# Kernel optimization log

Measured on AMD Instinct MI355X. Metric: run time of the kernel, lower is better.

## Reference

```python
import jax, jax.numpy as jnp
import numpy as np

INPUT_SIZE = 256
HIDDEN_SIZE = 512


def setup_inputs() -> dict:
    key = jax.random.key(0)
    ks = jax.random.split(key, 8)
    N, L = 128, 1024
    bound_cell = 1.0 / np.sqrt(HIDDEN_SIZE)
    bound_fc = 1.0 / np.sqrt(HIDDEN_SIZE)
    u = lambda k, shape, b: jax.random.uniform(k, shape, jnp.float32, -b, b)
    return {
        "x": jax.random.normal(ks[0], (N, L, INPUT_SIZE), jnp.float32),
        "h": jnp.zeros((N, HIDDEN_SIZE), jnp.float32),
        "W_ih": u(ks[1], (HIDDEN_SIZE, INPUT_SIZE), bound_cell),
        "W_hh": u(ks[2], (HIDDEN_SIZE, HIDDEN_SIZE), bound_cell),
        "b_ih": u(ks[3], (HIDDEN_SIZE,), bound_cell),
        "b_hh": u(ks[4], (HIDDEN_SIZE,), bound_cell),
        "W_out": u(ks[5], (HIDDEN_SIZE, HIDDEN_SIZE), bound_fc),
        "b_out": u(ks[6], (HIDDEN_SIZE,), bound_fc),
    }


def reference(x, h, W_ih, W_hh, b_ih, b_hh, W_out, b_out):
    # Precompute input projections for all timesteps in one big GEMM: [N,L,H]
    xp = jnp.einsum("nli,hi->nlh", x, W_ih) + b_ih + b_hh

    def step(h, xp_t):
        h = jnp.tanh(xp_t + h @ W_hh.T)
        return h, None

    # scan over time: xp transposed to [L,N,H]
    h, _ = jax.lax.scan(step, h, jnp.swapaxes(xp, 0, 1))
    y = h @ W_out.T + b_out
    return (y, h)
```

## Files before the change

### kernel.cpp

```cpp
#include <hip/hip_runtime.h>

typedef _Float16 f16;
typedef _Float16 f16x2 __attribute__((ext_vector_type(2)));
typedef _Float16 f16x4 __attribute__((ext_vector_type(4)));
typedef _Float16 f16x8 __attribute__((ext_vector_type(8)));
typedef float    f32x4 __attribute__((ext_vector_type(4)));

static __device__ __forceinline__ float dot4(uint4 w, uint4 h, float acc) {
    acc = __builtin_amdgcn_fdot2(__builtin_bit_cast(f16x2, w.x), __builtin_bit_cast(f16x2, h.x), acc, false);
    acc = __builtin_amdgcn_fdot2(__builtin_bit_cast(f16x2, w.y), __builtin_bit_cast(f16x2, h.y), acc, false);
    acc = __builtin_amdgcn_fdot2(__builtin_bit_cast(f16x2, w.z), __builtin_bit_cast(f16x2, h.z), acc, false);
    acc = __builtin_amdgcn_fdot2(__builtin_bit_cast(f16x2, w.w), __builtin_bit_cast(f16x2, h.w), acc, false);
    return acc;
}

static __device__ __forceinline__ float dppx1(float v) {
    int r = __builtin_amdgcn_mov_dpp(__builtin_bit_cast(int, v), 0xB1, 0xF, 0xF, true);
    return __builtin_bit_cast(float, r);
}
static __device__ __forceinline__ float dppx2(float v) {
    int r = __builtin_amdgcn_mov_dpp(__builtin_bit_cast(int, v), 0x4E, 0xF, 0xF, true);
    return __builtin_bit_cast(float, r);
}

__global__ __launch_bounds__(256) void cvt_w(const float4* __restrict__ wih4,
                                             const float4* __restrict__ whh4,
                                             f16x4* __restrict__ wih16,
                                             f16x4* __restrict__ whh16) {
    int idx = blockIdx.x * 256 + threadIdx.x;
    if (idx < 32768) {
        float4 v = wih4[idx];
        wih16[idx] = (f16x4){(f16)v.x, (f16)v.y, (f16)v.z, (f16)v.w};
    } else if (idx < 98304) {
        int k = idx - 32768;
        float4 v = whh4[k];
        whh16[k] = (f16x4){(f16)v.x, (f16)v.y, (f16)v.z, (f16)v.w};
    }
}

__global__ __launch_bounds__(256) void gemm_xp(const float* __restrict__ x,
                                               const f16* __restrict__ wih,
                                               const float* __restrict__ bih,
                                               const float* __restrict__ bhh,
                                               f16* __restrict__ xp,
                                               int tc, int t0, int L) {
    __shared__ f16 As[128][48];
    __shared__ f16 Bs[128][48];
    int tid = threadIdx.x;
    int r = tid >> 1, kh = (tid & 1) * 16;

    long mbase = (long)blockIdx.x * 128;
    int jb = blockIdx.y * 128;
    long mp = mbase + r;
    int n = (int)(mp / tc);
    int trel = (int)(mp - (long)n * tc);
    const float* xrow = x + ((long)n * L + t0 + trel) * 256 + kh;
    const f16* wrow = wih + (jb + r) * 256 + kh;

    int w = tid >> 6, l = tid & 63, lr = l & 15, lk = l >> 4;
    int wm = w & 1, wn = w >> 1;

    f32x4 acc[4][4] = {};

    for (int kk = 0; kk < 256; kk += 32) {
        float4 a0 = *(const float4*)(xrow + kk);
        float4 a1 = *(const float4*)(xrow + kk + 4);
        float4 a2 = *(const float4*)(xrow + kk + 8);
        float4 a3 = *(const float4*)(xrow + kk + 12);
        uint4  b0 = *(const uint4*)(wrow + kk);
        uint4  b1 = *(const uint4*)(wrow + kk + 8);
        f16x8 ca = {(f16)a0.x,(f16)a0.y,(f16)a0.z,(f16)a0.w,(f16)a1.x,(f16)a1.y,(f16)a1.z,(f16)a1.w};
        f16x8 cb = {(f16)a2.x,(f16)a2.y,(f16)a2.z,(f16)a2.w,(f16)a3.x,(f16)a3.y,(f16)a3.z,(f16)a3.w};
        __syncthreads();
        *(f16x8*)&As[r][kh]     = ca;
        *(f16x8*)&As[r][kh + 8] = cb;
        *(uint4*)&Bs[r][kh]     = b0;
        *(uint4*)&Bs[r][kh + 8] = b1;
        __syncthreads();

        uint4 af[4], bf[4];
#pragma unroll
        for (int mi = 0; mi < 4; ++mi) af[mi] = *(const uint4*)&As[wm * 64 + mi * 16 + lr][lk * 8];
#pragma unroll
        for (int ni = 0; ni < 4; ++ni) bf[ni] = *(const uint4*)&Bs[wn * 64 + ni * 16 + lr][lk * 8];
#pragma unroll
        for (int mi = 0; mi < 4; ++mi)
#pragma unroll
            for (int ni = 0; ni < 4; ++ni)
                acc[mi][ni] = __builtin_amdgcn_mfma_f32_16x16x32_f16(
                    __builtin_bit_cast(f16x8, af[mi]), __builtin_bit_cast(f16x8, bf[ni]),
                    acc[mi][ni], 0, 0, 0);
    }

#pragma unroll
    for (int ni = 0; ni < 4; ++ni) {
        int j = jb + wn * 64 + ni * 16 + lr;
        float bias = bih[j] + bhh[j];
#pragma unroll
        for (int mi = 0; mi < 4; ++mi) {
            long row = mbase + wm * 64 + mi * 16 + lk * 4;
#pragma unroll
            for (int rr = 0; rr < 4; ++rr)
                xp[(row + rr) * 512 + j] = (f16)(acc[mi][ni][rr] + bias);
        }
    }
}

__global__ __launch_bounds__(1024) void rnn_seq(const f16* __restrict__ whh16,
                                                const f16* __restrict__ xp,
                                                const float* __restrict__ hin,
                                                float* __restrict__ out,
                                                const float* __restrict__ wout,
                                                const float* __restrict__ bout,
                                                int tc, int finalflag, int ytotal) {
    __shared__ uint4 WL[8192];
    __shared__ uint4 hbuf[2][80];

    const int tid = threadIdx.x;
    const int n = blockIdx.x;
    const int i  = tid & 15;
    const int jg = tid >> 4;
    const int sw = tid & 7;

    uint4 wr[8][3];
    const f16* wbase = whh16 + (long)(jg * 8) * 512 + i * 32;
#pragma unroll
    for (int r = 0; r < 8; ++r) {
        const uint4* p = (const uint4*)(wbase + (long)r * 512);
        wr[r][0] = p[0]; wr[r][1] = p[1]; wr[r][2] = p[2];
        WL[tid * 8 + (r ^ sw)] = p[3];
    }

    if (tid < 512) {
        int j = tid;
        ((f16*)&hbuf[0][0])[((j >> 5) * 5 + ((j >> 3) & 3)) * 8 + (j & 7)] =
            (f16)hin[n * 512 + j];
    }
    __syncthreads();

    const int jrow = ((i & 1) << 2) | (i & 2) | ((i >> 2) & 1);
    const int jfin = jg * 8 + jrow;
    const int widx = ((jfin >> 5) * 5 + ((jfin >> 3) & 3)) * 8 + (jfin & 7);
    const f16* xpp = xp + ((long)n * tc) * 512 + jfin;
    const int wbyte = tid * 128 + sw * 16;

    float lasth = 0.f;
    int cur = 0;

    for (int t = 0; t < tc; ++t) {
        float xv = (float)xpp[(long)t * 512];

        const uint4* hrow = &hbuf[cur][i * 5];
        uint4 hv0 = hrow[0], hv1 = hrow[1], hv2 = hrow[2], hv3 = hrow[3];

        float a[8];
#pragma unroll
        for (int r = 0; r < 8; ++r)
            a[r] = dot4(wr[r][2], hv2, dot4(wr[r][1], hv1, dot4(wr[r][0], hv0, 0.f)));
#pragma unroll
        for (int r = 0; r < 8; ++r) {
            uint4 wl = *(const uint4*)((const char*)WL + (wbyte ^ (r << 4)));
            a[r] = dot4(wl, hv3, a[r]);
        }

#pragma unroll
        for (int s = 0; s < 4; ++s) {
            float lo = a[s], hi = a[s + 4];
            float keep = (i & 1) ? hi : lo, send = (i & 1) ? lo : hi;
            a[s] = keep + dppx1(send);
        }
#pragma unroll
        for (int s = 0; s < 2; ++s) {
            float lo = a[s], hi = a[s + 2];
            float keep = (i & 2) ? hi : lo, send = (i & 2) ? lo : hi;
            a[s] = keep + dppx2(send);
        }
        {
            float lo = a[0], hi = a[1];
            float keep = (i & 4) ? hi : lo, send = (i & 4) ? lo : hi;
            a[0] = keep + __shfl_xor(send, 4);
        }
        a[0] += __shfl_xor(a[0], 8);

        float pre = a[0] + xv;
        pre = fminf(fmaxf(pre, -20.f), 20.f);
        float e = __expf(2.f * pre);
        float hn = 1.f - 2.f / (e + 1.f);
        lasth = hn;
        ((f16*)&hbuf[cur ^ 1][0])[widx] = (f16)hn;
        __syncthreads();
        cur ^= 1;
    }

    out[ytotal + n * 512 + jfin] = lasth;

    if (finalflag) {
        __syncthreads();
        float* hf = (float*)WL;
        hf[jfin] = lasth;
        __syncthreads();
        if (tid < 512) {
            int jy = tid;
            float acc = bout[jy];
            const float* wrp = wout + (long)jy * 512;
#pragma unroll 4
            for (int k = 0; k < 512; k += 8) {
                float4 w0 = *(const float4*)(wrp + k);
                float4 w1 = *(const float4*)(wrp + k + 4);
                float4 g0 = *(const float4*)(hf + k);
                float4 g1 = *(const float4*)(hf + k + 4);
                acc = fmaf(w0.x, g0.x, acc); acc = fmaf(w0.y, g0.y, acc);
                acc = fmaf(w0.z, g0.z, acc); acc = fmaf(w0.w, g0.w, acc);
                acc = fmaf(w1.x, g1.x, acc); acc = fmaf(w1.y, g1.y, acc);
                acc = fmaf(w1.z, g1.z, acc); acc = fmaf(w1.w, g1.w, acc);
            }
            out[n * 512 + jy] = acc;
        }
    }
}

extern "C" void kernel_launch(void* const* d_in, const int* in_sizes, int n_in,
                              void* d_out, int out_size, void* d_ws, size_t ws_size,
                              hipStream_t stream) {
    const float* x    = (const float*)d_in[0];
    const float* h0   = (const float*)d_in[1];
    const float* wih  = (const float*)d_in[2];
    const float* whh  = (const float*)d_in[3];
    const float* bih  = (const float*)d_in[4];
    const float* bhh  = (const float*)d_in[5];
    const float* wout = (const float*)d_in[6];
    const float* bout = (const float*)d_in[7];
    float* out = (float*)d_out;

    int N = in_sizes[1] / 512;
    int L = (int)((long)in_sizes[0] / ((long)N * 256));
    int ytotal = N * 512;

    char* ws = (char*)d_ws;
    f16* whh16 = (f16*)ws;
    f16* wih16 = (f16*)(ws + 524288);
    f16* xp    = (f16*)(ws + 786432);
    long per_t = (long)N * 512 * 2;
    long cap = (ws_size > 786432) ? (long)(ws_size - 786432) : 0;
    long Tc = cap / per_t;
    if (Tc > L) Tc = L;
    if (Tc < 1) Tc = 1;

    cvt_w<<<384, 256, 0, stream>>>((const float4*)wih, (const float4*)whh,
                                   (f16x4*)wih16, (f16x4*)whh16);

    for (int t0 = 0; t0 < L;) {
        int tc = (int)((L - t0 < Tc) ? (L - t0) : Tc);
        gemm_xp<<<dim3(tc, 4), 256, 0, stream>>>(x, wih16, bih, bhh, xp, tc, t0, L);
        const float* hsrc = (t0 == 0) ? h0 : (const float*)(out + ytotal);
        int fin = (t0 + tc == L) ? 1 : 0;
        rnn_seq<<<N, 1024, 0, stream>>>(whh16, xp, hsrc, out, wout, bout, tc, fin, ytotal);
        t0 += tc;
    }
}
```

Before: 1.997 ms.

## Shrink recurrent block to 256 threads with 16 rows per thread group

Each RNN sequence block now runs with 256 threads instead of 1024. Each 8-lane group covers 16 hidden rows, with more W_hh held in registers (96 uint4 per thread) and the remainder in LDS. The reduction tree grows a level, and each lane finishes two outputs with a packed xp load and a packed h store. The aim is cheaper per-step barriers and fewer waves synchronizing. The cost is much higher register pressure that may spill, and less parallelism per step.

```diff
diff --git a/kernel.cpp b/kernel.cpp
--- a/kernel.cpp
+++ b/kernel.cpp
@@ -106,101 +106,111 @@
     }
 }
 
-__global__ __launch_bounds__(1024) void rnn_seq(const f16* __restrict__ whh16,
-                                                const f16* __restrict__ xp,
-                                                const float* __restrict__ hin,
-                                                float* __restrict__ out,
-                                                const float* __restrict__ wout,
-                                                const float* __restrict__ bout,
-                                                int tc, int finalflag, int ytotal) {
+__global__ __launch_bounds__(256, 1) void rnn_seq(const f16* __restrict__ whh16,
+                                                  const f16* __restrict__ xp,
+                                                  const float* __restrict__ hin,
+                                                  float* __restrict__ out,
+                                                  const float* __restrict__ wout,
+                                                  const float* __restrict__ bout,
+                                                  int tc, int finalflag, int ytotal) {
     __shared__ uint4 WL[8192];
-    __shared__ uint4 hbuf[2][80];
+    __shared__ uint4 hb[2][64];
 
     const int tid = threadIdx.x;
     const int n = blockIdx.x;
-    const int i  = tid & 15;
-    const int jg = tid >> 4;
-    const int sw = tid & 7;
-
-    uint4 wr[8][3];
-    const f16* wbase = whh16 + (long)(jg * 8) * 512 + i * 32;
-#pragma unroll
-    for (int r = 0; r < 8; ++r) {
+    const int i  = tid & 7;
+    const int jg = tid >> 3;
+
+    uint4 wr[16][6];
+    const f16* wbase = whh16 + (long)(jg * 16) * 512 + i * 64;
+#pragma unroll
+    for (int r = 0; r < 16; ++r) {
         const uint4* p = (const uint4*)(wbase + (long)r * 512);
-        wr[r][0] = p[0]; wr[r][1] = p[1]; wr[r][2] = p[2];
-        WL[tid * 8 + (r ^ sw)] = p[3];
-    }
-
-    if (tid < 512) {
-        int j = tid;
-        ((f16*)&hbuf[0][0])[((j >> 5) * 5 + ((j >> 3) & 3)) * 8 + (j & 7)] =
-            (f16)hin[n * 512 + j];
+#pragma unroll
+        for (int c = 0; c < 6; ++c) wr[r][c] = p[c];
+        WL[(r * 2 + 0) * 256 + tid] = p[6];
+        WL[(r * 2 + 1) * 256 + tid] = p[7];
+    }
+
+    f16* hb0 = (f16*)&hb[0][0];
+#pragma unroll
+    for (int e = 0; e < 2; ++e) {
+        int j = tid * 2 + e;
+        int g = j >> 6, c = (j >> 3) & 7, p = j & 7;
+        hb0[(g * 8 + (c ^ g)) * 8 + p] = (f16)hin[n * 512 + j];
     }
     __syncthreads();
 
-    const int jrow = ((i & 1) << 2) | (i & 2) | ((i >> 2) & 1);
-    const int jfin = jg * 8 + jrow;
-    const int widx = ((jfin >> 5) * 5 + ((jfin >> 3) & 3)) * 8 + (jfin & 7);
-    const f16* xpp = xp + ((long)n * tc) * 512 + jfin;
-    const int wbyte = tid * 128 + sw * 16;
-
-    float lasth = 0.f;
+    const int jr0 = 8 * (i & 1) + 4 * ((i >> 1) & 1) + 2 * ((i >> 2) & 1);
+    const int j0 = jg * 16 + jr0;
+    const int wg0 = j0 >> 6, wc0 = (j0 >> 3) & 7, wp0 = j0 & 7;
+    const int hwidx = (wg0 * 8 + (wc0 ^ wg0)) * 8 + wp0;
+    const f16* xpp = xp + ((long)n * tc) * 512 + j0;
+
+    float h0f = 0.f, h1f = 0.f;
     int cur = 0;
 
     for (int t = 0; t < tc; ++t) {
-        float xv = (float)xpp[(long)t * 512];
-
-        const uint4* hrow = &hbuf[cur][i * 5];
-        uint4 hv0 = hrow[0], hv1 = hrow[1], hv2 = hrow[2], hv3 = hrow[3];
-
-        float a[8];
-#pragma unroll
-        for (int r = 0; r < 8; ++r)
-            a[r] = dot4(wr[r][2], hv2, dot4(wr[r][1], hv1, dot4(wr[r][0], hv0, 0.f)));
-#pragma unroll
-        for (int r = 0; r < 8; ++r) {
-            uint4 wl = *(const uint4*)((const char*)WL + (wbyte ^ (r << 4)));
-            a[r] = dot4(wl, hv3, a[r]);
-        }
-
+        unsigned xv2 = *(const unsigned*)(xpp + (long)t * 512);
+
+        const uint4* hc = &hb[cur][i * 8];
+        float a[16];
+
+        uint4 h0 = hc[0 ^ i], h1 = hc[1 ^ i], h2 = hc[2 ^ i], h3 = hc[3 ^ i];
+#pragma unroll
+        for (int r = 0; r < 16; ++r)
+            a[r] = dot4(wr[r][3], h3, dot4(wr[r][2], h2, dot4(wr[r][1], h1, dot4(wr[r][0], h0, 0.f))));
+        h0 = hc[4 ^ i]; h1 = hc[5 ^ i]; h2 = hc[6 ^ i]; h3 = hc[7 ^ i];
+#pragma unroll
+        for (int r = 0; r < 16; ++r) {
+            float v = dot4(wr[r][5], h1, dot4(wr[r][4], h0, a[r]));
+            v = dot4(WL[(r * 2 + 0) * 256 + tid], h2, v);
+            a[r] = dot4(WL[(r * 2 + 1) * 256 + tid], h3, v);
+        }
+
+#pragma unroll
+        for (int s = 0; s < 8; ++s) {
+            float lo = a[s], hi = a[s + 8];
+            float keep = (i & 1) ? hi : lo, send = (i & 1) ? lo : hi;
+            a[s] = keep + dppx1(send);
+        }
 #pragma unroll
         for (int s = 0; s < 4; ++s) {
             float lo = a[s], hi = a[s + 4];
-            float keep = (i & 1) ? hi : lo, send = (i & 1) ? lo : hi;
-            a[s] = keep + dppx1(send);
+            float keep = (i & 2) ? hi : lo, send = (i & 2) ? lo : hi;
+            a[s] = keep + dppx2(send);
         }
 #pragma unroll
         for (int s = 0; s < 2; ++s) {
             float lo = a[s], hi = a[s + 2];
-            float keep = (i & 2) ? hi : lo, send = (i & 2) ? lo : hi;
-            a[s] = keep + dppx2(send);
-        }
-        {
-            float lo = a[0], hi = a[1];
             float keep = (i & 4) ? hi : lo, send = (i & 4) ? lo : hi;
-            a[0] = keep + __shfl_xor(send, 4);
-        }
-        a[0] += __shfl_xor(a[0], 8);
-
-        float pre = a[0] + xv;
-        pre = fminf(fmaxf(pre, -20.f), 20.f);
-        float e = __expf(2.f * pre);
-        float hn = 1.f - 2.f / (e + 1.f);
-        lasth = hn;
-        ((f16*)&hbuf[cur ^ 1][0])[widx] = (f16)hn;
+            a[s] = keep + __shfl_xor(send, 4);
+        }
+
+        f16x2 xv = __builtin_bit_cast(f16x2, xv2);
+        float pre0 = a[0] + (float)xv.x;
+        float pre1 = a[1] + (float)xv.y;
+        pre0 = fminf(fmaxf(pre0, -20.f), 20.f);
+        pre1 = fminf(fmaxf(pre1, -20.f), 20.f);
+        h0f = 1.f - 2.f / (__expf(2.f * pre0) + 1.f);
+        h1f = 1.f - 2.f / (__expf(2.f * pre1) + 1.f);
+        f16x2 hx = {(f16)h0f, (f16)h1f};
+        *(f16x2*)&((f16*)&hb[cur ^ 1][0])[hwidx] = hx;
         __syncthreads();
         cur ^= 1;
     }
 
-    out[ytotal + n * 512 + jfin] = lasth;
+    out[ytotal + n * 512 + j0]     = h0f;
+    out[ytotal + n * 512 + j0 + 1] = h1f;
 
     if (finalflag) {
-        __syncthreads();
         float* hf = (float*)WL;
-        hf[jfin] = lasth;
-        __syncthreads();
-        if (tid < 512) {
-            int jy = tid;
+        hf[j0]     = h0f;
+        hf[j0 + 1] = h1f;
+        __syncthreads();
+#pragma unroll
+        for (int e = 0; e < 2; ++e) {
+            int jy = tid + e * 256;
             float acc = bout[jy];
             const float* wrp = wout + (long)jy * 512;
 #pragma unroll 4
@@ -254,7 +264,7 @@
         gemm_xp<<<dim3(tc, 4), 256, 0, stream>>>(x, wih16, bih, bhh, xp, tc, t0, L);
         const float* hsrc = (t0 == 0) ? h0 : (const float*)(out + ytotal);
         int fin = (t0 + tc == L) ? 1 : 0;
-        rnn_seq<<<N, 1024, 0, stream>>>(whh16, xp, hsrc, out, wout, bout, tc, fin, ytotal);
+        rnn_seq<<<N, 256, 0, stream>>>(whh16, xp, hsrc, out, wout, bout, tc, fin, ytotal);
         t0 += tc;
     }
 }
```

New measurement: 3.046 ms. 52.5% more time.

## Halve RNN recurrence block to 512 threads with 8-lane K split

Applied to the files above, without the earlier changes.

The sequential recurrence kernel now uses 512 threads per sequence instead of 1024. Each thread covers 64 of the K dimension: 48 weights per row sit in registers and 16 in LDS, stored in a new transposed layout. This removes one cross-lane reduction stage and makes the per-step barrier cheaper, at the cost of twice the dot-product work per thread and higher register pressure. The h buffer layout changes to an XOR swizzle to avoid LDS bank conflicts.

```diff
diff --git a/kernel.cpp b/kernel.cpp
--- a/kernel.cpp
+++ b/kernel.cpp
@@ -106,43 +106,43 @@
     }
 }
 
-__global__ __launch_bounds__(1024) void rnn_seq(const f16* __restrict__ whh16,
-                                                const f16* __restrict__ xp,
-                                                const float* __restrict__ hin,
-                                                float* __restrict__ out,
-                                                const float* __restrict__ wout,
-                                                const float* __restrict__ bout,
-                                                int tc, int finalflag, int ytotal) {
-    __shared__ uint4 WL[8192];
-    __shared__ uint4 hbuf[2][80];
+__global__ __launch_bounds__(512, 1) void rnn_seq(const f16* __restrict__ whh16,
+                                                  const f16* __restrict__ xp,
+                                                  const float* __restrict__ hin,
+                                                  float* __restrict__ out,
+                                                  const float* __restrict__ wout,
+                                                  const float* __restrict__ bout,
+                                                  int tc, int finalflag, int ytotal) {
+    __shared__ uint4 WL[16 * 512];
+    __shared__ uint4 hb[2][64];
 
     const int tid = threadIdx.x;
     const int n = blockIdx.x;
-    const int i  = tid & 15;
-    const int jg = tid >> 4;
-    const int sw = tid & 7;
-
-    uint4 wr[8][3];
-    const f16* wbase = whh16 + (long)(jg * 8) * 512 + i * 32;
+    const int i  = tid & 7;
+    const int jg = tid >> 3;
+
+    uint4 wr[8][6];
+    const f16* wbase = whh16 + (long)(jg * 8) * 512 + i * 64;
 #pragma unroll
     for (int r = 0; r < 8; ++r) {
         const uint4* p = (const uint4*)(wbase + (long)r * 512);
-        wr[r][0] = p[0]; wr[r][1] = p[1]; wr[r][2] = p[2];
-        WL[tid * 8 + (r ^ sw)] = p[3];
-    }
-
-    if (tid < 512) {
+#pragma unroll
+        for (int c = 0; c < 6; ++c) wr[r][c] = p[c];
+        WL[(r * 2 + 0) * 512 + tid] = p[6];
+        WL[(r * 2 + 1) * 512 + tid] = p[7];
+    }
+
+    {
         int j = tid;
-        ((f16*)&hbuf[0][0])[((j >> 5) * 5 + ((j >> 3) & 3)) * 8 + (j & 7)] =
-            (f16)hin[n * 512 + j];
+        int g = j >> 6, c = (j >> 3) & 7, p = j & 7;
+        ((f16*)&hb[0][0])[(g * 8 + (c ^ g)) * 8 + p] = (f16)hin[n * 512 + j];
     }
     __syncthreads();
 
-    const int jrow = ((i & 1) << 2) | (i & 2) | ((i >> 2) & 1);
-    const int jfin = jg * 8 + jrow;
-    const int widx = ((jfin >> 5) * 5 + ((jfin >> 3) & 3)) * 8 + (jfin & 7);
+    const int jfin = jg * 8 + (((i & 1) << 2) | (i & 2) | ((i >> 2) & 1));
+    const int wg0 = jfin >> 6, wc0 = (jfin >> 3) & 7, wp0 = jfin & 7;
+    const int hwidx = (wg0 * 8 + (wc0 ^ wg0)) * 8 + wp0;
     const f16* xpp = xp + ((long)n * tc) * 512 + jfin;
-    const int wbyte = tid * 128 + sw * 16;
 
     float lasth = 0.f;
     int cur = 0;
@@ -150,17 +150,19 @@
     for (int t = 0; t < tc; ++t) {
         float xv = (float)xpp[(long)t * 512];
 
-        const uint4* hrow = &hbuf[cur][i * 5];
-        uint4 hv0 = hrow[0], hv1 = hrow[1], hv2 = hrow[2], hv3 = hrow[3];
-
+        const uint4* hc = &hb[cur][i * 8];
         float a[8];
+
+        uint4 h0 = hc[0 ^ i], h1 = hc[1 ^ i], h2 = hc[2 ^ i], h3 = hc[3 ^ i];
 #pragma unroll
         for (int r = 0; r < 8; ++r)
-            a[r] = dot4(wr[r][2], hv2, dot4(wr[r][1], hv1, dot4(wr[r][0], hv0, 0.f)));
+            a[r] = dot4(wr[r][3], h3, dot4(wr[r][2], h2, dot4(wr[r][1], h1, dot4(wr[r][0], h0, 0.f))));
+        h0 = hc[4 ^ i]; h1 = hc[5 ^ i]; h2 = hc[6 ^ i]; h3 = hc[7 ^ i];
 #pragma unroll
         for (int r = 0; r < 8; ++r) {
-            uint4 wl = *(const uint4*)((const char*)WL + (wbyte ^ (r << 4)));
-            a[r] = dot4(wl, hv3, a[r]);
+            float v = dot4(wr[r][5], h1, dot4(wr[r][4], h0, a[r]));
+            v = dot4(WL[(r * 2 + 0) * 512 + tid], h2, v);
+            a[r] = dot4(WL[(r * 2 + 1) * 512 + tid], h3, v);
         }
 
 #pragma unroll
@@ -180,14 +182,13 @@
             float keep = (i & 4) ? hi : lo, send = (i & 4) ? lo : hi;
             a[0] = keep + __shfl_xor(send, 4);
         }
-        a[0] += __shfl_xor(a[0], 8);
 
         float pre = a[0] + xv;
         pre = fminf(fmaxf(pre, -20.f), 20.f);
         float e = __expf(2.f * pre);
         float hn = 1.f - 2.f / (e + 1.f);
         lasth = hn;
-        ((f16*)&hbuf[cur ^ 1][0])[widx] = (f16)hn;
+        ((f16*)&hb[cur ^ 1][0])[hwidx] = (f16)hn;
         __syncthreads();
         cur ^= 1;
     }
@@ -195,27 +196,24 @@
     out[ytotal + n * 512 + jfin] = lasth;
 
     if (finalflag) {
-        __syncthreads();
         float* hf = (float*)WL;
         hf[jfin] = lasth;
         __syncthreads();
-        if (tid < 512) {
-            int jy = tid;
-            float acc = bout[jy];
-            const float* wrp = wout + (long)jy * 512;
+        int jy = tid;
+        float acc = bout[jy];
+        const float* wrp = wout + (long)jy * 512;
 #pragma unroll 4
-            for (int k = 0; k < 512; k += 8) {
-                float4 w0 = *(const float4*)(wrp + k);
-                float4 w1 = *(const float4*)(wrp + k + 4);
-                float4 g0 = *(const float4*)(hf + k);
-                float4 g1 = *(const float4*)(hf + k + 4);
-                acc = fmaf(w0.x, g0.x, acc); acc = fmaf(w0.y, g0.y, acc);
-                acc = fmaf(w0.z, g0.z, acc); acc = fmaf(w0.w, g0.w, acc);
-                acc = fmaf(w1.x, g1.x, acc); acc = fmaf(w1.y, g1.y, acc);
-                acc = fmaf(w1.z, g1.z, acc); acc = fmaf(w1.w, g1.w, acc);
-            }
-            out[n * 512 + jy] = acc;
-        }
+        for (int k = 0; k < 512; k += 8) {
+            float4 w0 = *(const float4*)(wrp + k);
+            float4 w1 = *(const float4*)(wrp + k + 4);
+            float4 g0 = *(const float4*)(hf + k);
+            float4 g1 = *(const float4*)(hf + k + 4);
+            acc = fmaf(w0.x, g0.x, acc); acc = fmaf(w0.y, g0.y, acc);
+            acc = fmaf(w0.z, g0.z, acc); acc = fmaf(w0.w, g0.w, acc);
+            acc = fmaf(w1.x, g1.x, acc); acc = fmaf(w1.y, g1.y, acc);
+            acc = fmaf(w1.z, g1.z, acc); acc = fmaf(w1.w, g1.w, acc);
+        }
+        out[n * 512 + jy] = acc;
     }
 }
 
@@ -254,7 +252,7 @@
         gemm_xp<<<dim3(tc, 4), 256, 0, stream>>>(x, wih16, bih, bhh, xp, tc, t0, L);
         const float* hsrc = (t0 == 0) ? h0 : (const float*)(out + ytotal);
         int fin = (t0 + tc == L) ? 1 : 0;
-        rnn_seq<<<N, 1024, 0, stream>>>(whh16, xp, hsrc, out, wout, bout, tc, fin, ytotal);
+        rnn_seq<<<N, 512, 0, stream>>>(whh16, xp, hsrc, out, wout, bout, tc, fin, ytotal);
         t0 += tc;
     }
 }
```

Result: faster. 1.778 ms (-10.9%).
